# Performance work log

Hardware: AMD Instinct MI355X
Metric: run time of the kernel (lower is better)

## Reference

```python
import jax, jax.numpy as jnp
import numpy as np


def setup_inputs() -> dict:
    key = jax.random.key(0)
    k1, k2, k3, k4 = jax.random.split(key, 4)
    B, T, C, H = 16, 2048, 384, 64
    x = jax.random.normal(k1, (B, T, C), dtype=jnp.float32)
    Wq = jax.random.normal(k2, (C, H), dtype=jnp.float32) * (1.0 / np.sqrt(C))
    Wk = jax.random.normal(k3, (C, H), dtype=jnp.float32) * (1.0 / np.sqrt(C))
    Wv = jax.random.normal(k4, (C, H), dtype=jnp.float32) * (1.0 / np.sqrt(C))
    return {"x": x, "Wq": Wq, "Wk": Wk, "Wv": Wv}


def reference(x, Wq, Wk, Wv):
    # x: [B, T, C]; Wq/Wk/Wv: [C, H]
    T = x.shape[1]
    H = Wk.shape[1]
    q = jnp.einsum('btc,ch->bth', x, Wq)
    k = jnp.einsum('btc,ch->bth', x, Wk)
    v = jnp.einsum('btc,ch->bth', x, Wv)
    scale = 1.0 / jnp.sqrt(jnp.asarray(H, dtype=x.dtype))
    wei = jnp.einsum('bth,bsh->bts', q, k) * scale  # [B, T, T]
    causal = jnp.tril(jnp.ones((T, T), dtype=bool))
    wei = jnp.where(causal, wei, -jnp.inf)
    attn = jax.nn.softmax(wei, axis=-1)
    # dropout p=0 -> identity
    out = jnp.einsum('bts,bsh->bth', attn, v)  # [B, T, H]
    return out
```

## Files before the change

kernel.cpp:

```cpp
#include <hip/hip_runtime.h>
#include <hip/hip_bf16.h>

#define B_ 16
#define T_ 2048
#define C_ 384
#define H_ 64

typedef __attribute__((ext_vector_type(8))) short short8;
typedef __attribute__((ext_vector_type(4))) short short4_t;
typedef __attribute__((ext_vector_type(4))) float floatx4;
typedef __attribute__((ext_vector_type(2))) unsigned int uint2_t;
typedef __attribute__((ext_vector_type(4))) unsigned int uintx4;

#if defined(__has_builtin)
#if __has_builtin(__builtin_amdgcn_mfma_f32_16x16x16bf16_1k)
#define HAVE_MFMA16 1
#endif
#endif

static __device__ __forceinline__ short f2bf(float f) {
    unsigned u = __builtin_bit_cast(unsigned, f);
    u += 0x7FFF + ((u >> 16) & 1);
    return (short)(u >> 16);
}
static __device__ __forceinline__ float bf2f(short s) {
    return __builtin_bit_cast(float, ((unsigned)(unsigned short)s) << 16);
}
static __device__ __forceinline__ unsigned cvt_pk_bf16(float lo, float hi) {
    unsigned r;
    asm("v_cvt_pk_bf16_f32 %0, %1, %2" : "=v"(r) : "v"(lo), "v"(hi));
    return r;
}

__global__ void wt_kernel(const float* __restrict__ Wq, const float* __restrict__ Wk,
                          const float* __restrict__ Wv, short* __restrict__ wt2) {
    int idx = blockIdx.x * 256 + threadIdx.x;
    if (idx >= 12 * 12 * 512) return;
    int f = idx >> 9, within = idx & 511;
    int lane = within >> 3, jj = within & 7;
    int nt16 = f / 12, kc32 = f - nt16 * 12;
    int mat = nt16 >> 2, w = nt16 & 3;
    int quad = lane >> 4, l16 = lane & 15;
    int h = w * 16 + l16;
    int c = kc32 * 32 + quad * 8 + jj;
    const float* W = (mat == 0) ? Wq : ((mat == 1) ? Wk : Wv);
    wt2[idx] = f2bf(W[c * H_ + h]);
}

__global__ __launch_bounds__(256) void qkv_kernel(
        const float* __restrict__ x, const short* __restrict__ wt2,
        short* __restrict__ qo, short* __restrict__ ko, short* __restrict__ vto) {
    __shared__ short xs[32 * 392];

    int b = blockIdx.y, t0 = blockIdx.x * 32;
    int tid = threadIdx.x;

    const float* src = x + (size_t)(b * T_ + t0) * C_;
    for (int i = 0; i < 12; i++) {
        int chunk = i * 256 + tid;
        int row = chunk / 96, off = (chunk % 96) * 4;
        float4 f = *(const float4*)&src[row * 384 + off];
        uint2_t u2;
        u2.x = cvt_pk_bf16(f.x, f.y);
        u2.y = cvt_pk_bf16(f.z, f.w);
        *(uint2_t*)&xs[row * 392 + off] = u2;
    }
    __syncthreads();

    int w = tid >> 6, lane = tid & 63, quad = lane >> 4, l16 = lane & 15;

    floatx4 acc[2][3];
    for (int mt = 0; mt < 2; mt++)
        for (int j = 0; j < 3; j++) acc[mt][j] = (floatx4)0.0f;

    for (int kc = 0; kc < 384; kc += 32) {
        int kc32 = kc >> 5;
        short8 a0 = *(const short8*)&xs[l16 * 392 + kc + quad * 8];
        short8 a1 = *(const short8*)&xs[(16 + l16) * 392 + kc + quad * 8];
        for (int j = 0; j < 3; j++) {
            short8 bf = *(const short8*)&wt2[(((j * 4 + w) * 12) + kc32) * 512 + lane * 8];
            acc[0][j] = __builtin_amdgcn_mfma_f32_16x16x32_bf16(a0, bf, acc[0][j], 0, 0, 0);
            acc[1][j] = __builtin_amdgcn_mfma_f32_16x16x32_bf16(a1, bf, acc[1][j], 0, 0, 0);
        }
    }
    __syncthreads();

    {
        int h = w * 16 + l16;
        for (int j = 0; j < 3; j++)
            for (int mt = 0; mt < 2; mt++)
                for (int r = 0; r < 4; r += 2) {
                    unsigned pk2 = cvt_pk_bf16(acc[mt][j][r], acc[mt][j][r + 1]);
                    int tl0 = mt * 16 + quad * 4 + r;
                    if (j == 0) {
                        xs[tl0 * 72 + h] = (short)pk2;
                        xs[(tl0 + 1) * 72 + h] = (short)(pk2 >> 16);
                    } else if (j == 1) {
                        xs[2304 + tl0 * 72 + h] = (short)pk2;
                        xs[2304 + (tl0 + 1) * 72 + h] = (short)(pk2 >> 16);
                    } else {
                        *(unsigned*)&xs[4608 + h * 40 + tl0] = pk2;
                    }
                }
    }
    __syncthreads();

    {
        int row = tid >> 3, off = (tid & 7) * 8;
        *(short8*)&qo[(size_t)(b * T_ + t0 + row) * H_ + off] = *(const short8*)&xs[row * 72 + off];
        *(short8*)&ko[(size_t)(b * T_ + t0 + row) * H_ + off] = *(const short8*)&xs[2304 + row * 72 + off];
    }
    {
        int h = tid >> 2, off = (tid & 3) * 8;
        *(short8*)&vto[(size_t)(b * H_ + h) * T_ + t0 + off] = *(const short8*)&xs[4608 + h * 40 + off];
    }
}

#define KVSZ (64 * 72)
#define SLOT_BYTES (16384 + 512)

__global__ __launch_bounds__(256) void attn_seg_kernel(
        const short* __restrict__ q, const short* __restrict__ k,
        const short* __restrict__ vt, float* __restrict__ slots) {
    __shared__ short ks[2 * KVSZ];
    __shared__ short vs[2 * KVSZ];
#if !defined(HAVE_MFMA16)
    __shared__ short ps[4 * 16 * 72];
#endif

    int b = blockIdx.y, fid = blockIdx.x, nslot = gridDim.x;
    int tt = 0, cum = 0;
    while (cum + ((2 * tt + 5) >> 2) <= fid) { cum += (2 * tt + 5) >> 2; tt++; }
    int nk = 2 * tt + 2;
    int k0 = (fid - cum) * 4;
    int k1 = min(k0 + 4, nk);

    int tid = threadIdx.x, w = tid >> 6, lane = tid & 63, quad = lane >> 4, l16 = lane & 15;
    int trow0 = tt * 128 + w * 32;

    short8 aq[2][2];
    for (int mt = 0; mt < 2; mt++) {
        const short* qrow = q + (size_t)(b * T_ + trow0 + mt * 16 + l16) * H_;
        aq[mt][0] = *(const short8*)&qrow[quad * 8];
        aq[mt][1] = *(const short8*)&qrow[32 + quad * 8];
    }

    floatx4 o[2][4];
    for (int mt = 0; mt < 2; mt++)
        for (int i = 0; i < 4; i++) o[mt][i] = (floatx4)0.0f;
    float lp[2] = {0.f, 0.f};

    const short* kb0 = k + (size_t)b * T_ * H_;
    const short* vtb = vt + (size_t)b * H_ * T_;

    int srow = tid >> 3, soff = (tid & 7) * 8;
    const float C1 = 0.125f * 1.44269504f;
    const float C2 = 12.0f * 1.44269504f;

    {
        const short* kg = kb0 + (size_t)k0 * 64 * H_;
        const short* vg = vtb + k0 * 64;
        *(short8*)&ks[srow * 72 + soff] = *(const short8*)&kg[srow * H_ + soff];
        *(short8*)&ks[(srow + 32) * 72 + soff] = *(const short8*)&kg[(srow + 32) * H_ + soff];
        *(short8*)&vs[srow * 72 + soff] = *(const short8*)&vg[(size_t)srow * T_ + soff];
        *(short8*)&vs[(srow + 32) * 72 + soff] = *(const short8*)&vg[(size_t)(srow + 32) * T_ + soff];
    }
    __syncthreads();

    int p = 0;
    for (int st = k0; st < k1; st++) {
        bool more = (st + 1 < k1);
        short8 pk0, pk1, pv0, pv1;
        if (more) {
            const short* kg = kb0 + (size_t)(st + 1) * 64 * H_;
            const short* vg = vtb + (st + 1) * 64;
            pk0 = *(const short8*)&kg[srow * H_ + soff];
            pk1 = *(const short8*)&kg[(srow + 32) * H_ + soff];
            pv0 = *(const short8*)&vg[(size_t)srow * T_ + soff];
            pv1 = *(const short8*)&vg[(size_t)(srow + 32) * T_ + soff];
        }
        const short* ksp = ks + p * KVSZ;
        const short* vsp = vs + p * KVSZ;
        int s0 = st * 64;

        floatx4 sacc[2][4];
        for (int mt = 0; mt < 2; mt++)
            for (int nt = 0; nt < 4; nt++) sacc[mt][nt] = (floatx4)0.0f;
        for (int nt = 0; nt < 4; nt++) {
            short8 bk0 = *(const short8*)&ksp[(nt * 16 + l16) * 72 + quad * 8];
            short8 bk1 = *(const short8*)&ksp[(nt * 16 + l16) * 72 + 32 + quad * 8];
            sacc[0][nt] = __builtin_amdgcn_mfma_f32_16x16x32_bf16(bk0, aq[0][0], sacc[0][nt], 0, 0, 0);
            sacc[0][nt] = __builtin_amdgcn_mfma_f32_16x16x32_bf16(bk1, aq[0][1], sacc[0][nt], 0, 0, 0);
            sacc[1][nt] = __builtin_amdgcn_mfma_f32_16x16x32_bf16(bk0, aq[1][0], sacc[1][nt], 0, 0, 0);
            sacc[1][nt] = __builtin_amdgcn_mfma_f32_16x16x32_bf16(bk1, aq[1][1], sacc[1][nt], 0, 0, 0);
        }

        bool diag = (st >= 2 * tt);
#if defined(HAVE_MFMA16)
        short4_t pa[2][4];
        for (int mt = 0; mt < 2; mt++) {
            int q_idx = trow0 + mt * 16 + l16;
            for (int nt = 0; nt < 4; nt++) {
                float pv[4];
                for (int r = 0; r < 4; r++) {
                    float pe = __builtin_amdgcn_exp2f(fmaf(sacc[mt][nt][r], C1, -C2));
                    int s_idx = s0 + nt * 16 + quad * 4 + r;
                    if (diag && (s_idx > q_idx)) pe = 0.0f;
                    lp[mt] += pe;
                    pv[r] = pe;
                }
                uint2_t u;
                u.x = cvt_pk_bf16(pv[0], pv[1]);
                u.y = cvt_pk_bf16(pv[2], pv[3]);
                pa[mt][nt] = __builtin_bit_cast(short4_t, u);
            }
        }
        for (int nh = 0; nh < 4; nh++) {
            const short* vrow = &vsp[(nh * 16 + l16) * 72 + quad * 4];
            for (int c = 0; c < 4; c++) {
                short4_t bv = *(const short4_t*)&vrow[c * 16];
                o[0][nh] = __builtin_amdgcn_mfma_f32_16x16x16bf16_1k(pa[0][c], bv, o[0][nh], 0, 0, 0);
                o[1][nh] = __builtin_amdgcn_mfma_f32_16x16x16bf16_1k(pa[1][c], bv, o[1][nh], 0, 0, 0);
            }
        }
#else
        short* psw = ps + w * 16 * 72;
        short8 ap[2][2];
        for (int mt = 0; mt < 2; mt++) {
            int q_idx = trow0 + mt * 16 + l16;
            for (int nt = 0; nt < 4; nt++)
                for (int r = 0; r < 4; r++) {
                    float pv = __builtin_amdgcn_exp2f(fmaf(sacc[mt][nt][r], C1, -C2));
                    int s_idx = s0 + nt * 16 + quad * 4 + r;
                    if (diag && (s_idx > q_idx)) pv = 0.0f;
                    lp[mt] += pv;
                    psw[l16 * 72 + nt * 16 + quad * 4 + r] = f2bf(pv);
                }
            ap[mt][0] = *(const short8*)&psw[l16 * 72 + quad * 8];
            ap[mt][1] = *(const short8*)&psw[l16 * 72 + 32 + quad * 8];
        }
        for (int nh = 0; nh < 4; nh++) {
            short8 bv0 = *(const short8*)&vsp[(nh * 16 + l16) * 72 + quad * 8];
            short8 bv1 = *(const short8*)&vsp[(nh * 16 + l16) * 72 + 32 + quad * 8];
            o[0][nh] = __builtin_amdgcn_mfma_f32_16x16x32_bf16(ap[0][0], bv0, o[0][nh], 0, 0, 0);
            o[0][nh] = __builtin_amdgcn_mfma_f32_16x16x32_bf16(ap[0][1], bv1, o[0][nh], 0, 0, 0);
            o[1][nh] = __builtin_amdgcn_mfma_f32_16x16x32_bf16(ap[1][0], bv0, o[1][nh], 0, 0, 0);
            o[1][nh] = __builtin_amdgcn_mfma_f32_16x16x32_bf16(ap[1][1], bv1, o[1][nh], 0, 0, 0);
        }
#endif

        if (more) {
            short* kd = ks + (1 - p) * KVSZ;
            short* vd = vs + (1 - p) * KVSZ;
            *(short8*)&kd[srow * 72 + soff] = pk0;
            *(short8*)&kd[(srow + 32) * 72 + soff] = pk1;
            *(short8*)&vd[srow * 72 + soff] = pv0;
            *(short8*)&vd[(srow + 32) * 72 + soff] = pv1;
            __syncthreads();
            p ^= 1;
        }
    }

    for (int mt = 0; mt < 2; mt++) {
        lp[mt] += __shfl_xor(lp[mt], 16);
        lp[mt] += __shfl_xor(lp[mt], 32);
    }

    char* slotb = (char*)slots + ((size_t)b * nslot + fid) * SLOT_BYTES;
    short* slotO = (short*)slotb;
    float* slotL = (float*)(slotb + 16384);

    for (int mt = 0; mt < 2; mt++)
        for (int nh = 0; nh < 4; nh++)
            for (int r = 0; r < 4; r += 2) {
                unsigned pk2 = cvt_pk_bf16(o[mt][nh][r], o[mt][nh][r + 1]);
                slotO[(w * 32 + mt * 16 + quad * 4 + r) * 64 + nh * 16 + l16] = (short)pk2;
                slotO[(w * 32 + mt * 16 + quad * 4 + r + 1) * 64 + nh * 16 + l16] = (short)(pk2 >> 16);
            }
    if (quad == 0)
        for (int mt = 0; mt < 2; mt++)
            slotL[w * 32 + mt * 16 + l16] = lp[mt];
}

__global__ __launch_bounds__(256) void combine_kernel(
        const float* __restrict__ slots, int nslot, float* __restrict__ out) {
    int b = blockIdx.y, tb = blockIdx.x;
    int tt = tb >> 1;
    int nseg = (2 * tt + 5) >> 2;
    int cum = 0;
    for (int i = 0; i < tt; i++) cum += (2 * i + 5) >> 2;
    const char* base = (const char*)slots + ((size_t)b * nslot + cum) * SLOT_BYTES;

    int tid = threadIdx.x;
    int row = (tb & 1) * 64 + (tid >> 2);
    int qo = (tid & 3) * 16;
    float acc[16];
    for (int i = 0; i < 16; i++) acc[i] = 0.f;
    float lsum = 0.f;
    for (int s = 0; s < nseg; s++) {
        const short* O = (const short*)(base + (size_t)s * SLOT_BYTES);
        const float* L = (const float*)(base + (size_t)s * SLOT_BYTES + 16384);
        for (int i = 0; i < 2; i++) {
            short8 v = *(const short8*)&O[row * 64 + qo + i * 8];
            uintx4 u = __builtin_bit_cast(uintx4, v);
            for (int j = 0; j < 4; j++) {
                acc[i * 8 + 2 * j]     += __builtin_bit_cast(float, u[j] << 16);
                acc[i * 8 + 2 * j + 1] += __builtin_bit_cast(float, u[j] & 0xFFFF0000u);
            }
        }
        lsum += L[row];
    }
    float inv = 1.0f / lsum;
    float* op = out + (size_t)(b * T_ + tt * 128 + row) * H_ + qo;
    for (int i = 0; i < 4; i++) {
        float4 v;
        v.x = acc[i * 4 + 0] * inv; v.y = acc[i * 4 + 1] * inv;
        v.z = acc[i * 4 + 2] * inv; v.w = acc[i * 4 + 3] * inv;
        *(float4*)&op[i * 4] = v;
    }
}

template<bool DIAG>
static __device__ __forceinline__ void attn_step(
        int s0, int t0w, int quad, int l16,
        const short* __restrict__ kbase, const short* __restrict__ vtb,
        short8 aq0, short8 aq1, short* __restrict__ psw,
        floatx4 (&o)[4], float (&lpart)[4]) {
    floatx4 sacc[4];
    for (int nt = 0; nt < 4; nt++) sacc[nt] = (floatx4)0.0f;
    for (int nt = 0; nt < 4; nt++) {
        short8 bk0 = *(const short8*)&kbase[(nt * 16 + l16) * H_ + quad * 8];
        short8 bk1 = *(const short8*)&kbase[(nt * 16 + l16) * H_ + 32 + quad * 8];
        sacc[nt] = __builtin_amdgcn_mfma_f32_16x16x32_bf16(aq0, bk0, sacc[nt], 0, 0, 0);
        sacc[nt] = __builtin_amdgcn_mfma_f32_16x16x32_bf16(aq1, bk1, sacc[nt], 0, 0, 0);
    }
    const float C1 = 0.125f * 1.44269504f;
    const float C2 = 12.0f * 1.44269504f;
    for (int nt = 0; nt < 4; nt++) {
        int s_idx = s0 + nt * 16 + l16;
        for (int r = 0; r < 4; r++) {
            float p = __builtin_amdgcn_exp2f(fmaf(sacc[nt][r], C1, -C2));
            if (DIAG && (s_idx > t0w + quad * 4 + r)) p = 0.0f;
            lpart[r] += p;
            psw[(quad * 4 + r) * 72 + nt * 16 + l16] = f2bf(p);
        }
    }
    short8 ap0 = *(const short8*)&psw[l16 * 72 + quad * 8];
    short8 ap1 = *(const short8*)&psw[l16 * 72 + 32 + quad * 8];
    for (int nh = 0; nh < 4; nh++) {
        short8 bv0 = *(const short8*)&vtb[(size_t)(nh * 16 + l16) * T_ + s0 + quad * 8];
        short8 bv1 = *(const short8*)&vtb[(size_t)(nh * 16 + l16) * T_ + s0 + 32 + quad * 8];
        o[nh] = __builtin_amdgcn_mfma_f32_16x16x32_bf16(ap0, bv0, o[nh], 0, 0, 0);
        o[nh] = __builtin_amdgcn_mfma_f32_16x16x32_bf16(ap1, bv1, o[nh], 0, 0, 0);
    }
}

__global__ __launch_bounds__(256) void attn_kernel(
        const short* __restrict__ q, const short* __restrict__ k,
        const short* __restrict__ vt, float* __restrict__ out) {
    __shared__ short ps[4 * 16 * 72];

    int b = blockIdx.y;
    int g = ((int)blockIdx.x + 4 * (b & 7)) & 31;
    int tt = (b < 8) ? g : 31 - g;
    int t0 = tt * 64;
    int tid = threadIdx.x, w = tid >> 6, lane = tid & 63, quad = lane >> 4, l16 = lane & 15;
    int t0w = t0 + w * 16;

    const short* qrow = q + (size_t)(b * T_ + t0w + l16) * H_;
    short8 aq0 = *(const short8*)&qrow[quad * 8];
    short8 aq1 = *(const short8*)&qrow[32 + quad * 8];

    floatx4 o[4];
    for (int nh = 0; nh < 4; nh++) o[nh] = (floatx4)0.0f;
    float lpart[4] = {0.f, 0.f, 0.f, 0.f};

    const short* kb0 = k + (size_t)b * T_ * H_;
    const short* vtb = vt + (size_t)b * H_ * T_;
    short* psw = ps + w * 16 * 72;

    for (int st = 0; st < tt; st++)
        attn_step<false>(st * 64, t0w, quad, l16, kb0 + (size_t)st * 64 * H_,
                         vtb, aq0, aq1, psw, o, lpart);
    attn_step<true>(tt * 64, t0w, quad, l16, kb0 + (size_t)tt * 64 * H_,
                    vtb, aq0, aq1, psw, o, lpart);

    for (int d = 1; d < 16; d <<= 1)
        for (int r = 0; r < 4; r++)
            lpart[r] += __shfl_xor(lpart[r], d, 16);

    for (int nh = 0; nh < 4; nh++)
        for (int r = 0; r < 4; r++) {
            int t = t0w + quad * 4 + r;
            out[(size_t)(b * T_ + t) * H_ + nh * 16 + l16] = o[nh][r] / lpart[r];
        }
}

extern "C" void kernel_launch(void* const* d_in, const int* in_sizes, int n_in,
                              void* d_out, int out_size, void* d_ws, size_t ws_size,
                              hipStream_t stream) {
    const float* x  = (const float*)d_in[0];
    const float* Wq = (const float*)d_in[1];
    const float* Wk = (const float*)d_in[2];
    const float* Wv = (const float*)d_in[3];

    char* ws = (char*)d_ws;
    short* qb  = (short*)(ws);
    short* kb  = (short*)(ws + (size_t)4 * 1024 * 1024);
    short* vtb = (short*)(ws + (size_t)8 * 1024 * 1024);
    short* wtb = (short*)(ws + (size_t)12 * 1024 * 1024);
    float* slots = (float*)(ws + (size_t)12 * 1024 * 1024 + 256 * 1024);
    size_t base_need = (size_t)12 * 1024 * 1024 + 256 * 1024;

    wt_kernel<<<dim3(288), dim3(256), 0, stream>>>(Wq, Wk, Wv, wtb);
    qkv_kernel<<<dim3(T_ / 32, B_), dim3(256), 0, stream>>>(x, wtb, qb, kb, vtb);

    float* out = (float*)d_out;
    const int NSLOT = 72;
    if (ws_size >= base_need + (size_t)B_ * NSLOT * (size_t)SLOT_BYTES) {
        attn_seg_kernel<<<dim3(NSLOT, B_), dim3(256), 0, stream>>>(qb, kb, vtb, slots);
        combine_kernel<<<dim3(T_ / 64, B_), dim3(256), 0, stream>>>(slots, NSLOT, out);
    } else {
        attn_kernel<<<dim3(T_ / 64, B_), dim3(256), 0, stream>>>(qb, kb, vtb, out);
    }
}
```

Measured before the change: 133.8 us.

## Fuse split-KV combine into attention via atomic last-block reduction; enlarge QKV tile

```diff
diff --git a/kernel.cpp b/kernel.cpp
--- a/kernel.cpp
+++ b/kernel.cpp
@@ -33,7 +33,9 @@
 }
 
 __global__ void wt_kernel(const float* __restrict__ Wq, const float* __restrict__ Wk,
-                          const float* __restrict__ Wv, short* __restrict__ wt2) {
+                          const float* __restrict__ Wv, short* __restrict__ wt2,
+                          unsigned* __restrict__ counters) {
+    if (blockIdx.x == 0 && threadIdx.x < B_ * 16) counters[threadIdx.x] = 0u;
     int idx = blockIdx.x * 256 + threadIdx.x;
     if (idx >= 12 * 12 * 512) return;
     int f = idx >> 9, within = idx & 511;
@@ -50,13 +52,13 @@
 __global__ __launch_bounds__(256) void qkv_kernel(
         const float* __restrict__ x, const short* __restrict__ wt2,
         short* __restrict__ qo, short* __restrict__ ko, short* __restrict__ vto) {
-    __shared__ short xs[32 * 392];
-
-    int b = blockIdx.y, t0 = blockIdx.x * 32;
+    __shared__ short xs[64 * 392];
+
+    int b = blockIdx.y, t0 = blockIdx.x * 64;
     int tid = threadIdx.x;
 
     const float* src = x + (size_t)(b * T_ + t0) * C_;
-    for (int i = 0; i < 12; i++) {
+    for (int i = 0; i < 24; i++) {
         int chunk = i * 256 + tid;
         int row = chunk / 96, off = (chunk % 96) * 4;
         float4 f = *(const float4*)&src[row * 384 + off];
@@ -69,18 +71,19 @@
 
     int w = tid >> 6, lane = tid & 63, quad = lane >> 4, l16 = lane & 15;
 
-    floatx4 acc[2][3];
-    for (int mt = 0; mt < 2; mt++)
+    floatx4 acc[4][3];
+    for (int mt = 0; mt < 4; mt++)
         for (int j = 0; j < 3; j++) acc[mt][j] = (floatx4)0.0f;
 
     for (int kc = 0; kc < 384; kc += 32) {
         int kc32 = kc >> 5;
-        short8 a0 = *(const short8*)&xs[l16 * 392 + kc + quad * 8];
-        short8 a1 = *(const short8*)&xs[(16 + l16) * 392 + kc + quad * 8];
+        short8 a[4];
+        for (int mt = 0; mt < 4; mt++)
+            a[mt] = *(const short8*)&xs[(mt * 16 + l16) * 392 + kc + quad * 8];
         for (int j = 0; j < 3; j++) {
             short8 bf = *(const short8*)&wt2[(((j * 4 + w) * 12) + kc32) * 512 + lane * 8];
-            acc[0][j] = __builtin_amdgcn_mfma_f32_16x16x32_bf16(a0, bf, acc[0][j], 0, 0, 0);
-            acc[1][j] = __builtin_amdgcn_mfma_f32_16x16x32_bf16(a1, bf, acc[1][j], 0, 0, 0);
+            for (int mt = 0; mt < 4; mt++)
+                acc[mt][j] = __builtin_amdgcn_mfma_f32_16x16x32_bf16(a[mt], bf, acc[mt][j], 0, 0, 0);
         }
     }
     __syncthreads();
@@ -88,7 +91,7 @@
     {
         int h = w * 16 + l16;
         for (int j = 0; j < 3; j++)
-            for (int mt = 0; mt < 2; mt++)
+            for (int mt = 0; mt < 4; mt++)
                 for (int r = 0; r < 4; r += 2) {
                     unsigned pk2 = cvt_pk_bf16(acc[mt][j][r], acc[mt][j][r + 1]);
                     int tl0 = mt * 16 + quad * 4 + r;
@@ -96,10 +99,10 @@
                         xs[tl0 * 72 + h] = (short)pk2;
                         xs[(tl0 + 1) * 72 + h] = (short)(pk2 >> 16);
                     } else if (j == 1) {
-                        xs[2304 + tl0 * 72 + h] = (short)pk2;
-                        xs[2304 + (tl0 + 1) * 72 + h] = (short)(pk2 >> 16);
+                        xs[4608 + tl0 * 72 + h] = (short)pk2;
+                        xs[4608 + (tl0 + 1) * 72 + h] = (short)(pk2 >> 16);
                     } else {
-                        *(unsigned*)&xs[4608 + h * 40 + tl0] = pk2;
+                        *(unsigned*)&xs[9216 + h * 72 + tl0] = pk2;
                     }
                 }
     }
@@ -107,12 +110,16 @@
 
     {
         int row = tid >> 3, off = (tid & 7) * 8;
-        *(short8*)&qo[(size_t)(b * T_ + t0 + row) * H_ + off] = *(const short8*)&xs[row * 72 + off];
-        *(short8*)&ko[(size_t)(b * T_ + t0 + row) * H_ + off] = *(const short8*)&xs[2304 + row * 72 + off];
+        for (int i = 0; i < 2; i++) {
+            int rr = row + i * 32;
+            *(short8*)&qo[(size_t)(b * T_ + t0 + rr) * H_ + off] = *(const short8*)&xs[rr * 72 + off];
+            *(short8*)&ko[(size_t)(b * T_ + t0 + rr) * H_ + off] = *(const short8*)&xs[4608 + rr * 72 + off];
+        }
     }
     {
-        int h = tid >> 2, off = (tid & 3) * 8;
-        *(short8*)&vto[(size_t)(b * H_ + h) * T_ + t0 + off] = *(const short8*)&xs[4608 + h * 40 + off];
+        int h = tid >> 2, off = (tid & 3) * 16;
+        *(short8*)&vto[(size_t)(b * H_ + h) * T_ + t0 + off] = *(const short8*)&xs[9216 + h * 72 + off];
+        *(short8*)&vto[(size_t)(b * H_ + h) * T_ + t0 + off + 8] = *(const short8*)&xs[9216 + h * 72 + off + 8];
     }
 }
 
@@ -121,9 +128,11 @@
 
 __global__ __launch_bounds__(256) void attn_seg_kernel(
         const short* __restrict__ q, const short* __restrict__ k,
-        const short* __restrict__ vt, float* __restrict__ slots) {
+        const short* __restrict__ vt, float* __restrict__ slots,
+        unsigned* __restrict__ counters, float* __restrict__ out) {
     __shared__ short ks[2 * KVSZ];
     __shared__ short vs[2 * KVSZ];
+    __shared__ unsigned last_flag;
 #if !defined(HAVE_MFMA16)
     __shared__ short ps[4 * 16 * 72];
 #endif
@@ -132,6 +141,7 @@
     int tt = 0, cum = 0;
     while (cum + ((2 * tt + 5) >> 2) <= fid) { cum += (2 * tt + 5) >> 2; tt++; }
     int nk = 2 * tt + 2;
+    int nseg = (2 * tt + 5) >> 2;
     int k0 = (fid - cum) * 4;
     int k1 = min(k0 + 4, nk);
 
@@ -280,43 +290,42 @@
     if (quad == 0)
         for (int mt = 0; mt < 2; mt++)
             slotL[w * 32 + mt * 16 + l16] = lp[mt];
-}
-
-__global__ __launch_bounds__(256) void combine_kernel(
-        const float* __restrict__ slots, int nslot, float* __restrict__ out) {
-    int b = blockIdx.y, tb = blockIdx.x;
-    int tt = tb >> 1;
-    int nseg = (2 * tt + 5) >> 2;
-    int cum = 0;
-    for (int i = 0; i < tt; i++) cum += (2 * i + 5) >> 2;
-    const char* base = (const char*)slots + ((size_t)b * nslot + cum) * SLOT_BYTES;
-
-    int tid = threadIdx.x;
-    int row = (tb & 1) * 64 + (tid >> 2);
-    int qo = (tid & 3) * 16;
-    float acc[16];
-    for (int i = 0; i < 16; i++) acc[i] = 0.f;
-    float lsum = 0.f;
-    for (int s = 0; s < nseg; s++) {
-        const short* O = (const short*)(base + (size_t)s * SLOT_BYTES);
-        const float* L = (const float*)(base + (size_t)s * SLOT_BYTES + 16384);
-        for (int i = 0; i < 2; i++) {
-            short8 v = *(const short8*)&O[row * 64 + qo + i * 8];
-            uintx4 u = __builtin_bit_cast(uintx4, v);
-            for (int j = 0; j < 4; j++) {
-                acc[i * 8 + 2 * j]     += __builtin_bit_cast(float, u[j] << 16);
-                acc[i * 8 + 2 * j + 1] += __builtin_bit_cast(float, u[j] & 0xFFFF0000u);
+
+    __syncthreads();
+    if (tid == 0) {
+        __threadfence();
+        unsigned old = atomicAdd(&counters[b * 16 + tt], 1u);
+        last_flag = (old == (unsigned)(nseg - 1)) ? 1u : 0u;
+    }
+    __syncthreads();
+    if (last_flag) {
+        __threadfence();
+        const char* cbase = (const char*)slots + ((size_t)b * nslot + cum) * SLOT_BYTES;
+        int row = tid >> 1, half = tid & 1;
+        float facc[32];
+        for (int i = 0; i < 32; i++) facc[i] = 0.f;
+        float lsum = 0.f;
+        for (int s = 0; s < nseg; s++) {
+            const short* O = (const short*)(cbase + (size_t)s * SLOT_BYTES);
+            const float* L = (const float*)(cbase + (size_t)s * SLOT_BYTES + 16384);
+            for (int i = 0; i < 4; i++) {
+                short8 v = *(const short8*)&O[row * 64 + half * 32 + i * 8];
+                uintx4 u = __builtin_bit_cast(uintx4, v);
+                for (int j = 0; j < 4; j++) {
+                    facc[i * 8 + 2 * j]     += __builtin_bit_cast(float, u[j] << 16);
+                    facc[i * 8 + 2 * j + 1] += __builtin_bit_cast(float, u[j] & 0xFFFF0000u);
+                }
             }
-        }
-        lsum += L[row];
-    }
-    float inv = 1.0f / lsum;
-    float* op = out + (size_t)(b * T_ + tt * 128 + row) * H_ + qo;
-    for (int i = 0; i < 4; i++) {
-        float4 v;
-        v.x = acc[i * 4 + 0] * inv; v.y = acc[i * 4 + 1] * inv;
-        v.z = acc[i * 4 + 2] * inv; v.w = acc[i * 4 + 3] * inv;
-        *(float4*)&op[i * 4] = v;
+            lsum += L[row];
+        }
+        float inv = 1.0f / lsum;
+        float* op = out + (size_t)(b * T_ + tt * 128 + row) * H_ + half * 32;
+        for (int i = 0; i < 8; i++) {
+            float4 v;
+            v.x = facc[i * 4 + 0] * inv; v.y = facc[i * 4 + 1] * inv;
+            v.z = facc[i * 4 + 2] * inv; v.w = facc[i * 4 + 3] * inv;
+            *(float4*)&op[i * 4] = v;
+        }
     }
 }
 
@@ -409,17 +418,19 @@
     short* kb  = (short*)(ws + (size_t)4 * 1024 * 1024);
     short* vtb = (short*)(ws + (size_t)8 * 1024 * 1024);
     short* wtb = (short*)(ws + (size_t)12 * 1024 * 1024);
-    float* slots = (float*)(ws + (size_t)12 * 1024 * 1024 + 256 * 1024);
-    size_t base_need = (size_t)12 * 1024 * 1024 + 256 * 1024;
-
-    wt_kernel<<<dim3(288), dim3(256), 0, stream>>>(Wq, Wk, Wv, wtb);
-    qkv_kernel<<<dim3(T_ / 32, B_), dim3(256), 0, stream>>>(x, wtb, qb, kb, vtb);
+    const int NSLOT = 72;
+    size_t slots_off = (size_t)12 * 1024 * 1024 + 256 * 1024;
+    size_t slots_bytes = (size_t)B_ * NSLOT * (size_t)SLOT_BYTES;
+    float* slots = (float*)(ws + slots_off);
+    unsigned* counters = (unsigned*)(ws + slots_off + slots_bytes);
+    size_t base_need = slots_off + slots_bytes + B_ * 16 * sizeof(unsigned);
+
+    wt_kernel<<<dim3(288), dim3(256), 0, stream>>>(Wq, Wk, Wv, wtb, counters);
+    qkv_kernel<<<dim3(T_ / 64, B_), dim3(256), 0, stream>>>(x, wtb, qb, kb, vtb);
 
     float* out = (float*)d_out;
-    const int NSLOT = 72;
-    if (ws_size >= base_need + (size_t)B_ * NSLOT * (size_t)SLOT_BYTES) {
-        attn_seg_kernel<<<dim3(NSLOT, B_), dim3(256), 0, stream>>>(qb, kb, vtb, slots);
-        combine_kernel<<<dim3(T_ / 64, B_), dim3(256), 0, stream>>>(slots, NSLOT, out);
+    if (ws_size >= base_need) {
+        attn_seg_kernel<<<dim3(NSLOT, B_), dim3(256), 0, stream>>>(qb, kb, vtb, slots, counters, out);
     } else {
         attn_kernel<<<dim3(T_ / 64, B_), dim3(256), 0, stream>>>(qb, kb, vtb, out);
     }
```

New measurement: 276.5 us. 2.07x slower.
